# Performance work log

Hardware: AMD Instinct MI355X
Metric: run time of the kernel (lower is better)

## Reference

```python
import jax, jax.numpy as jnp
import numpy as np

EPS = 1e-5
GROUPS = 32
HEADS = 8
RES_SCALE = 0.7071067811865476  # 1/sqrt(2)


def group_norm(x, groups, weight=None, bias=None):
    # x: [b, c, t]; normalize over (c//groups, t) per group, like torch GroupNorm
    b, c, t = x.shape
    xg = x.reshape(b, groups, (c // groups) * t)
    mean = xg.mean(axis=-1, keepdims=True)
    var = xg.var(axis=-1, keepdims=True)
    xg = (xg - mean) * jax.lax.rsqrt(var + EPS)
    x = xg.reshape(b, c, t)
    if weight is not None:
        x = x * weight[None, :, None] + bias[None, :, None]
    return x


def setup_inputs() -> dict:
    key = jax.random.key(0)
    ks = jax.random.split(key, 7)
    b, c, hh, ww = 8, 512, 32, 32
    return {
        "x": jax.random.normal(ks[0], (b, c, hh, ww), dtype=jnp.float32),
        "gn_w": jax.random.uniform(ks[1], (c,), dtype=jnp.float32, minval=0.5, maxval=1.5),
        "gn_b": jax.random.normal(ks[2], (c,), dtype=jnp.float32) * 0.1,
        "qkv_w": jax.random.normal(ks[3], (3 * c, c), dtype=jnp.float32) * (c ** -0.5),
        "qkv_b": jax.random.normal(ks[4], (3 * c,), dtype=jnp.float32) * 0.02,
        "proj_w": jax.random.normal(ks[5], (c, c), dtype=jnp.float32) * 0.02,
        "proj_b": jax.random.normal(ks[6], (c,), dtype=jnp.float32) * 0.02,
    }


def reference(x, gn_w, gn_b, qkv_w, qkv_b, proj_w, proj_b):
    b, c, hh, ww = x.shape
    t = hh * ww
    ch = c // HEADS
    xf = x.reshape(b, c, t)
    xn = group_norm(xf, GROUPS, gn_w, gn_b)
    # 1x1 conv -> GEMM: [b, 3c, t]
    qkv = jnp.einsum('oc,bct->bot', qkv_w, xn) + qkv_b[None, :, None]
    # split order: per head contiguous [q_ch; k_ch; v_ch]
    qkv = qkv.reshape(b * HEADS, 3 * ch, t)
    q, k, v = jnp.split(qkv, 3, axis=1)
    scale = ch ** -0.25
    w = jnp.einsum('bct,bcs->bts', q * scale, k * scale)
    w = jax.nn.softmax(w.astype(jnp.float32), axis=-1).astype(qkv.dtype)
    a = jnp.einsum('bts,bcs->bct', w, v).reshape(b, c, t)
    h = jnp.einsum('oc,bct->bot', proj_w, a) + proj_b[None, :, None]
    out = group_norm(RES_SCALE * xn + h, GROUPS)  # functional group_norm: no affine
    return out.reshape(b, c, hh, ww)
```

## Files before the change

### kernel.cpp

```cpp
#include <hip/hip_runtime.h>


typedef unsigned short u16;
typedef __attribute__((ext_vector_type(8))) short short8v;
typedef __attribute__((ext_vector_type(4))) float float4v;

constexpr int NB = 8, NC = 512, NT = 1024, CPG = 16;
#define EPSV 1e-5f
#define RES_SCALE 0.7071067811865476f
#define QK_SCALE 0.35355339059327376f
#define LOG2E 1.4426950408889634f

static __device__ __forceinline__ u16 f2bf(float f) {
  unsigned int u = __builtin_bit_cast(unsigned int, f);
  u = (u + 0x7fffu + ((u >> 16) & 1u)) >> 16;
  return (u16)u;
}
static __device__ __forceinline__ float exp2_fast(float x) {
  float r;
  asm("v_exp_f32 %0, %1" : "=v"(r) : "v"(x));
  return r;
}
static __device__ __forceinline__ unsigned cvt_pk_bf16(float lo, float hi) {
  unsigned r;
  asm("v_cvt_pk_bf16_f32 %0, %1, %2" : "=v"(r) : "v"(lo), "v"(hi));
  return r;
}

__global__ __launch_bounds__(256) void gn1_prep_kernel(
    const float* __restrict__ x, const float* __restrict__ gw,
    const float* __restrict__ gb, float* __restrict__ xn, u16* __restrict__ xbt,
    const float* __restrict__ qw, const float* __restrict__ pw,
    u16* __restrict__ qwb, u16* __restrict__ pwb)
{
  __shared__ __attribute__((aligned(16))) u16 T[1024 * 24];
  __shared__ float rs[4], rq[4], stats[2];
  const int blk = blockIdx.x;
  const int tid = threadIdx.x;
  if (blk >= 256) {
    const int i = (blk - 256) * 256 + tid;
    const float* in; u16* out; int j;
    if (i < 98304) { in = qw; out = qwb; j = i; }
    else           { in = pw; out = pwb; j = i - 98304; }
    const float4 a = *(const float4*)(in + (size_t)j * 8);
    const float4 b = *(const float4*)(in + (size_t)j * 8 + 4);
    short8v o;
    o[0] = (short)f2bf(a.x); o[1] = (short)f2bf(a.y);
    o[2] = (short)f2bf(a.z); o[3] = (short)f2bf(a.w);
    o[4] = (short)f2bf(b.x); o[5] = (short)f2bf(b.y);
    o[6] = (short)f2bf(b.z); o[7] = (short)f2bf(b.w);
    *(short8v*)(out + (size_t)j * 8) = o;
    return;
  }
  const int b = blk >> 5, g = blk & 31;
  const size_t off = ((size_t)(b * NC + g * CPG)) * NT;
  const float4* s4 = (const float4*)(x + off);
  float sum = 0.f, sq = 0.f;
  #pragma unroll 4
  for (int i = tid; i < CPG * NT / 4; i += 256) {
    float4 v = s4[i];
    sum += v.x + v.y + v.z + v.w;
    sq  += v.x * v.x + v.y * v.y + v.z * v.z + v.w * v.w;
  }
  #pragma unroll
  for (int off2 = 32; off2; off2 >>= 1) {
    sum += __shfl_xor(sum, off2);
    sq  += __shfl_xor(sq,  off2);
  }
  const int wave = tid >> 6, lane = tid & 63;
  if (lane == 0) { rs[wave] = sum; rq[wave] = sq; }
  __syncthreads();
  if (tid == 0) {
    float S = rs[0] + rs[1] + rs[2] + rs[3];
    float Q = rq[0] + rq[1] + rq[2] + rq[3];
    float mean = S * (1.0f / (CPG * NT));
    float var  = Q * (1.0f / (CPG * NT)) - mean * mean;
    stats[0] = mean;
    stats[1] = rsqrtf(var + EPSV);
  }
  __syncthreads();
  const float mean = stats[0], rstd = stats[1];
  float4* d4 = (float4*)(xn + off);
  #pragma unroll 4
  for (int i = tid; i < CPG * NT / 4; i += 256) {
    const int ch = i >> 8;
    const float wv = gw[g * CPG + ch];
    const float a = rstd * wv;
    const float c2 = gb[g * CPG + ch] - mean * a;
    float4 v = s4[i];
    v.x = v.x * a + c2; v.y = v.y * a + c2;
    v.z = v.z * a + c2; v.w = v.w * a + c2;
    d4[i] = v;
    const int t4 = (i & 255) * 4;
    T[(t4 + 0) * 24 + ch] = f2bf(v.x);
    T[(t4 + 1) * 24 + ch] = f2bf(v.y);
    T[(t4 + 2) * 24 + ch] = f2bf(v.z);
    T[(t4 + 3) * 24 + ch] = f2bf(v.w);
  }
  __syncthreads();
  #pragma unroll
  for (int tt = 0; tt < 4; tt++) {
    const int t = tid + 256 * tt;
    uint4 lo = *(const uint4*)&T[t * 24];
    uint4 hi = *(const uint4*)&T[t * 24 + 8];
    u16* dst = xbt + ((size_t)b * NT + t) * NC + g * CPG;
    *(uint4*)dst = lo;
    *(uint4*)(dst + 8) = hi;
  }
}

template<int MODE>
__global__ __launch_bounds__(256) void mfma_gemm_kernel(
    const u16* __restrict__ Wb, const float* __restrict__ bias,
    const u16* __restrict__ Bt, u16* __restrict__ qkT,
    u16* __restrict__ vN, float* __restrict__ outF,
    const float* __restrict__ xnf)
{
  __shared__ __attribute__((aligned(16))) u16 lds[(MODE == 1) ? 17408 : 16384];
  const int tid = threadIdx.x;
  const int w = tid >> 6, l = tid & 63, lr = l & 15, lg = l >> 4;
  const int wm = (w >> 1) * 64, wn = (w & 1) * 64;
  const int bn = blockIdx.x * 128, bm = blockIdx.y * 128, b = blockIdx.z;

  const u16* Ag = Wb + (size_t)bm * 512;
  const u16* Bg = Bt + ((size_t)b * NT + bn) * 512;

  const int srow = w * 16 + (l >> 2);
  const int scg  = (l & 3) ^ ((l >> 3) & 3);
  const u16* ap0 = Ag + (size_t)srow * 512 + scg * 8;
  const u16* bp0 = Bg + (size_t)srow * 512 + scg * 8;
  char* ldsb = (char*)lds;
  char* adst0 = ldsb + w * 1024;

  float4v acc[4][4];
  #pragma unroll
  for (int i = 0; i < 4; i++)
    #pragma unroll
    for (int j = 0; j < 4; j++) acc[i][j] = (float4v){0.f, 0.f, 0.f, 0.f};

  #pragma unroll
  for (int r = 0; r < 2; r++) {
    __builtin_amdgcn_global_load_lds(ap0 + r * 64 * 512, adst0 + r * 4096, 16, 0, 0);
    __builtin_amdgcn_global_load_lds(bp0 + r * 64 * 512, adst0 + 8192 + r * 4096, 16, 0, 0);
  }
  asm volatile("s_waitcnt vmcnt(0)" ::: "memory");
  __builtin_amdgcn_s_barrier();

  for (int ks = 0; ks < 16; ++ks) {
    const int buf = ks & 1;
    if (ks < 15) {
      const size_t k0n = (size_t)(ks + 1) * 32;
      char* an = ldsb + (buf ^ 1) * 16384 + w * 1024;
      #pragma unroll
      for (int r = 0; r < 2; r++) {
        __builtin_amdgcn_global_load_lds(ap0 + k0n + r * 64 * 512, an + r * 4096, 16, 0, 0);
        __builtin_amdgcn_global_load_lds(bp0 + k0n + r * 64 * 512, an + 8192 + r * 4096, 16, 0, 0);
      }
    }
    const u16* au = lds + buf * 8192;
    const u16* bu = au + 4096;
    short8v af[4], bf[4];
    #pragma unroll
    for (int mi = 0; mi < 4; mi++) {
      const int m = wm + mi * 16 + lr;
      af[mi] = *(const short8v*)(au + m * 32 + ((lg ^ ((m >> 1) & 3)) * 8));
    }
    #pragma unroll
    for (int ni = 0; ni < 4; ni++) {
      const int n = wn + ni * 16 + lr;
      bf[ni] = *(const short8v*)(bu + n * 32 + ((lg ^ ((n >> 1) & 3)) * 8));
    }
    #pragma unroll
    for (int mi = 0; mi < 4; mi++)
      #pragma unroll
      for (int ni = 0; ni < 4; ni++)
        acc[mi][ni] = __builtin_amdgcn_mfma_f32_16x16x32_bf16(af[mi], bf[ni], acc[mi][ni], 0, 0, 0);
    if (ks < 15) {
      asm volatile("s_waitcnt vmcnt(0)" ::: "memory");
      __builtin_amdgcn_s_barrier();
    }
  }

  if (MODE == 0) {
    #pragma unroll
    for (int mi = 0; mi < 4; mi++) {
      const int m0 = bm + wm + mi * 16 + lg * 4;
      const int head = m0 / 192;
      const int r0 = m0 - head * 192;
      const float4 bv4 = *(const float4*)(bias + m0);
      if (r0 < 128) {
        const float scl = (r0 < 64) ? QK_SCALE * LOG2E : QK_SCALE;
        const int col = head * 128 + r0;
        #pragma unroll
        for (int ni = 0; ni < 4; ni++) {
          const int t = bn + wn + ni * 16 + lr;
          unsigned int lo = (unsigned)f2bf((acc[mi][ni][0] + bv4.x) * scl) |
                            ((unsigned)f2bf((acc[mi][ni][1] + bv4.y) * scl) << 16);
          unsigned int hi = (unsigned)f2bf((acc[mi][ni][2] + bv4.z) * scl) |
                            ((unsigned)f2bf((acc[mi][ni][3] + bv4.w) * scl) << 16);
          *(uint2*)(qkT + ((size_t)b * NT + t) * 1024 + col) = make_uint2(lo, hi);
        }
      } else {
        const int vc = head * 64 + (r0 - 128);
        #pragma unroll
        for (int ni = 0; ni < 4; ni++) {
          const int t = bn + wn + ni * 16 + lr;
          vN[((size_t)b * NC + vc + 0) * NT + t] = f2bf(acc[mi][ni][0] + bv4.x);
          vN[((size_t)b * NC + vc + 1) * NT + t] = f2bf(acc[mi][ni][1] + bv4.y);
          vN[((size_t)b * NC + vc + 2) * NT + t] = f2bf(acc[mi][ni][2] + bv4.z);
          vN[((size_t)b * NC + vc + 3) * NT + t] = f2bf(acc[mi][ni][3] + bv4.w);
        }
      }
    }
  } else {
    float* Cs = (float*)lds;
    for (int ph = 0; ph < 2; ph++) {
      __syncthreads();
      if ((w >> 1) == ph) {
        #pragma unroll
        for (int mi = 0; mi < 4; mi++)
          #pragma unroll
          for (int ni = 0; ni < 4; ni++) {
            const int rr = mi * 16 + lg * 4;
            const int cc2 = wn + ni * 16 + lr;
            #pragma unroll
            for (int r = 0; r < 4; r++)
              Cs[(rr + r) * 136 + cc2] = acc[mi][ni][r];
          }
      }
      __syncthreads();
      const int mloc = tid >> 2;
      const int m = bm + ph * 64 + mloc;
      const float bv = bias[m];
      const int cb = (tid & 3) * 32;
      const float* cr = Cs + mloc * 136 + cb;
      const float* xr = xnf + ((size_t)b * NC + m) * NT + bn + cb;
      float* yr = outF + ((size_t)b * NC + m) * NT + bn + cb;
      #pragma unroll
      for (int j = 0; j < 8; j++) {
        float4 c4 = *(const float4*)(cr + j * 4);
        float4 x4 = *(const float4*)(xr + j * 4);
        float4 o;
        o.x = c4.x + bv + RES_SCALE * x4.x;
        o.y = c4.y + bv + RES_SCALE * x4.y;
        o.z = c4.z + bv + RES_SCALE * x4.z;
        o.w = c4.w + bv + RES_SCALE * x4.w;
        *(float4*)(yr + j * 4) = o;
      }
    }
  }
}

__global__ __launch_bounds__(256) void groupnorm2_kernel(float* __restrict__ dst0)
{
  const int tid = threadIdx.x;
  const int b = blockIdx.x >> 5;
  const int g = blockIdx.x & 31;
  const size_t off = ((size_t)(b * NC + g * CPG)) * NT;
  float* dst = dst0 + off;
  const float4* s4 = (const float4*)dst;
  float sum = 0.f, sq = 0.f;
  #pragma unroll 4
  for (int i = tid; i < CPG * NT / 4; i += 256) {
    float4 v = s4[i];
    sum += v.x + v.y + v.z + v.w;
    sq  += v.x * v.x + v.y * v.y + v.z * v.z + v.w * v.w;
  }
  #pragma unroll
  for (int off2 = 32; off2; off2 >>= 1) {
    sum += __shfl_xor(sum, off2);
    sq  += __shfl_xor(sq,  off2);
  }
  __shared__ float rs[4], rq[4], stats[2];
  const int wave = tid >> 6, lane = tid & 63;
  if (lane == 0) { rs[wave] = sum; rq[wave] = sq; }
  __syncthreads();
  if (tid == 0) {
    float S = rs[0] + rs[1] + rs[2] + rs[3];
    float Q = rq[0] + rq[1] + rq[2] + rq[3];
    float mean = S * (1.0f / (CPG * NT));
    float var  = Q * (1.0f / (CPG * NT)) - mean * mean;
    stats[0] = mean;
    stats[1] = rsqrtf(var + EPSV);
  }
  __syncthreads();
  const float mean = stats[0], rstd = stats[1];
  float4* d4 = (float4*)dst;
  #pragma unroll 4
  for (int i = tid; i < CPG * NT / 4; i += 256) {
    float4 v = s4[i];
    const float c2 = -mean * rstd;
    v.x = v.x * rstd + c2; v.y = v.y * rstd + c2;
    v.z = v.z * rstd + c2; v.w = v.w * rstd + c2;
    d4[i] = v;
  }
}

__global__ __launch_bounds__(256, 4) void attn_mfma_kernel(
    const u16* __restrict__ qkT, const u16* __restrict__ vN, u16* __restrict__ aT)
{
  __shared__ __attribute__((aligned(16))) u16 lds[5 * 4096];
  const int tid = threadIdx.x;
  const int w = tid >> 6, l = tid & 63, lr = l & 15, lg = l >> 4;
  const int L = blockIdx.x;
  const int bh = (L & 7) * 8 + ((L >> 3) & 7);
  const int t0 = (L >> 6) * 64;
  const int b = bh >> 3, h = bh & 7;

  const u16* qbase = qkT + (size_t)b * NT * 1024 + h * 128;
  const u16* kbase = qbase + 64;
  const u16* vbase = vN + ((size_t)b * NC + h * 64) * NT;

  const size_t qrow = (size_t)(t0 + w * 16 + lr) * 1024;
  const short8v qa0 = *(const short8v*)(qbase + qrow + lg * 8);
  const short8v qa1 = *(const short8v*)(qbase + qrow + 32 + lg * 8);

  const int strow = w * 8 + (l >> 3);
  const int scg = (l & 7) ^ (l >> 3);
  const u16* kp0 = kbase + (size_t)strow * 1024 + scg * 8;
  const u16* vp0 = vbase + (size_t)strow * 1024 + scg * 8;
  char* ldsb = (char*)lds;
  u16* Psw = lds + 16384 + (w * 16 + lr) * 64;
  const int sx = (lr & 7) << 3;

  float4v out[4];
  #pragma unroll
  for (int nc = 0; nc < 4; nc++) out[nc] = (float4v){0.f, 0.f, 0.f, 0.f};
  float psum = 0.f;

  #pragma unroll
  for (int r = 0; r < 2; r++) {
    __builtin_amdgcn_global_load_lds(kp0 + (size_t)r * 32 * 1024,
                                     ldsb + w * 1024 + r * 4096, 16, 0, 0);
    __builtin_amdgcn_global_load_lds(vp0 + (size_t)r * 32 * 1024,
                                     ldsb + 16384 + w * 1024 + r * 4096, 16, 0, 0);
  }
  asm volatile("s_waitcnt vmcnt(0)" ::: "memory");
  __builtin_amdgcn_s_barrier();

  for (int it = 0; it < 16; ++it) {
    const int buf = it & 1;
    if (it < 15) {
      const size_t s0n = (size_t)(it + 1) * 64;
      char* kd = ldsb + (buf ^ 1) * 8192 + w * 1024;
      char* vd = ldsb + 16384 + (buf ^ 1) * 8192 + w * 1024;
      #pragma unroll
      for (int r = 0; r < 2; r++) {
        __builtin_amdgcn_global_load_lds(kp0 + (s0n + r * 32) * 1024, kd + r * 4096, 16, 0, 0);
        __builtin_amdgcn_global_load_lds(vp0 + s0n + (size_t)r * 32 * 1024, vd + r * 4096, 16, 0, 0);
      }
    }
    const u16* Kc = lds + buf * 4096;
    const u16* Vc = lds + 8192 + buf * 4096;

    float4v sacc[4];
    #pragma unroll
    for (int n = 0; n < 4; n++) sacc[n] = (float4v){0.f, 0.f, 0.f, 0.f};
    __builtin_amdgcn_s_setprio(1);
    #pragma unroll
    for (int n = 0; n < 4; n++) {
      const int srow = n * 16 + lr;
      short8v kb0 = *(const short8v*)(Kc + srow * 64 + ((lg ^ (srow & 7)) * 8));
      short8v kb1 = *(const short8v*)(Kc + srow * 64 + (((4 + lg) ^ (srow & 7)) * 8));
      sacc[n] = __builtin_amdgcn_mfma_f32_16x16x32_bf16(kb0, qa0, sacc[n], 0, 0, 0);
      sacc[n] = __builtin_amdgcn_mfma_f32_16x16x32_bf16(kb1, qa1, sacc[n], 0, 0, 0);
    }
    __builtin_amdgcn_s_setprio(0);

    #pragma unroll
    for (int n = 0; n < 4; n++) {
      float p0 = exp2_fast(sacc[n][0]);
      float p1 = exp2_fast(sacc[n][1]);
      float p2 = exp2_fast(sacc[n][2]);
      float p3 = exp2_fast(sacc[n][3]);
      psum += (p0 + p1) + (p2 + p3);
      unsigned w0 = cvt_pk_bf16(p0, p1);
      unsigned w1 = cvt_pk_bf16(p2, p3);
      *(uint2*)(Psw + ((n * 16 + lg * 4) ^ sx)) = make_uint2(w0, w1);
    }

    __builtin_amdgcn_s_setprio(1);
    #pragma unroll
    for (int kc = 0; kc < 2; kc++) {
      short8v pb = *(const short8v*)(Psw + ((kc * 32 + lg * 8) ^ sx));
      #pragma unroll
      for (int nc = 0; nc < 4; nc++) {
        const int crow = nc * 16 + lr;
        short8v vb = *(const short8v*)(Vc + crow * 64 + (((kc * 4 + lg) ^ (crow & 7)) * 8));
        out[nc] = __builtin_amdgcn_mfma_f32_16x16x32_bf16(vb, pb, out[nc], 0, 0, 0);
      }
    }
    __builtin_amdgcn_s_setprio(0);

    if (it < 15) {
      asm volatile("s_waitcnt vmcnt(0)" ::: "memory");
      __builtin_amdgcn_s_barrier();
    }
  }

  psum += __shfl_xor(psum, 16);
  psum += __shfl_xor(psum, 32);
  const float inv = 1.0f / psum;

  __syncthreads();
  u16* At = lds;
  #pragma unroll
  for (int nc = 0; nc < 4; nc++) {
    unsigned w0 = cvt_pk_bf16(out[nc][0] * inv, out[nc][1] * inv);
    unsigned w1 = cvt_pk_bf16(out[nc][2] * inv, out[nc][3] * inv);
    *(uint2*)(At + (w * 16 + lr) * 80 + nc * 16 + lg * 4) = make_uint2(w0, w1);
  }
  __syncthreads();
  const int t = tid >> 2, cp = (tid & 3) * 2;
  u16* dst = aT + ((size_t)b * NT + t0 + t) * NC + h * 64;
  #pragma unroll
  for (int q = 0; q < 2; q++)
    *(short8v*)(dst + (cp + q) * 8) = *(const short8v*)(At + t * 80 + (cp + q) * 8);
}

extern "C" void kernel_launch(void* const* d_in, const int* in_sizes, int n_in,
                              void* d_out, int out_size, void* d_ws, size_t ws_size,
                              hipStream_t stream)
{
  const float* x      = (const float*)d_in[0];
  const float* gn_w   = (const float*)d_in[1];
  const float* gn_b   = (const float*)d_in[2];
  const float* qkv_w  = (const float*)d_in[3];
  const float* qkv_b  = (const float*)d_in[4];
  const float* proj_w = (const float*)d_in[5];
  const float* proj_b = (const float*)d_in[6];
  float* out = (float*)d_out;

  float* xn  = (float*)d_ws;
  u16* base16 = (u16*)(xn + (size_t)NB * NC * NT);
  u16* xbt = base16;
  u16* qkT = xbt + (size_t)NB * NT * NC;
  u16* vN  = qkT + (size_t)NB * NT * 1024;
  u16* aT  = vN + (size_t)NB * NC * NT;
  u16* qwb = aT + (size_t)NB * NT * NC;
  u16* pwb = qwb + 1536 * 512;

  gn1_prep_kernel<<<dim3(768), 256, 0, stream>>>(x, gn_w, gn_b, xn, xbt,
                                                 qkv_w, proj_w, qwb, pwb);
  mfma_gemm_kernel<0><<<dim3(8, 12, NB), 256, 0, stream>>>(qwb, qkv_b, xbt, qkT, vN, nullptr, nullptr);
  attn_mfma_kernel<<<dim3(1024), 256, 0, stream>>>(qkT, vN, aT);
  mfma_gemm_kernel<1><<<dim3(8, 4, NB), 256, 0, stream>>>(pwb, proj_b, aT, nullptr, nullptr, out, xn);
  groupnorm2_kernel<<<dim3(256), 256, 0, stream>>>(out);
}
```

Baseline: 159.9 us.

## Store residual xn in bf16 and widen attention blocks to 512 threads

The normalized input kept for the residual is now written as bf16 instead of fp32. This halves the write traffic in the first groupnorm kernel and the residual read traffic in the projection epilogue. The attention kernel now uses 512-thread blocks covering 128 query rows, so each K/V tile loaded into LDS is shared by twice as many waves and the grid is halved. The cost is some precision loss in the residual term and higher per-block register and LDS pressure under the new launch bounds. The epilogue and tail code after the attention main loop were not visible, so their consistency with the new tile size cannot be confirmed.

```diff
diff --git a/kernel.cpp b/kernel.cpp
--- a/kernel.cpp
+++ b/kernel.cpp
@@ -16,6 +16,10 @@
   u = (u + 0x7fffu + ((u >> 16) & 1u)) >> 16;
   return (u16)u;
 }
+static __device__ __forceinline__ float bf2f(short s) {
+  unsigned u = ((unsigned)(unsigned short)s) << 16;
+  return __builtin_bit_cast(float, u);
+}
 static __device__ __forceinline__ float exp2_fast(float x) {
   float r;
   asm("v_exp_f32 %0, %1" : "=v"(r) : "v"(x));
@@ -29,7 +33,7 @@
 
 __global__ __launch_bounds__(256) void gn1_prep_kernel(
     const float* __restrict__ x, const float* __restrict__ gw,
-    const float* __restrict__ gb, float* __restrict__ xn, u16* __restrict__ xbt,
+    const float* __restrict__ gb, u16* __restrict__ xnc, u16* __restrict__ xbt,
     const float* __restrict__ qw, const float* __restrict__ pw,
     u16* __restrict__ qwb, u16* __restrict__ pwb)
 {
@@ -80,7 +84,6 @@
   }
   __syncthreads();
   const float mean = stats[0], rstd = stats[1];
-  float4* d4 = (float4*)(xn + off);
   #pragma unroll 4
   for (int i = tid; i < CPG * NT / 4; i += 256) {
     const int ch = i >> 8;
@@ -90,7 +93,8 @@
     float4 v = s4[i];
     v.x = v.x * a + c2; v.y = v.y * a + c2;
     v.z = v.z * a + c2; v.w = v.w * a + c2;
-    d4[i] = v;
+    *(uint2*)(xnc + off + (size_t)i * 4) =
+        make_uint2(cvt_pk_bf16(v.x, v.y), cvt_pk_bf16(v.z, v.w));
     const int t4 = (i & 255) * 4;
     T[(t4 + 0) * 24 + ch] = f2bf(v.x);
     T[(t4 + 1) * 24 + ch] = f2bf(v.y);
@@ -114,7 +118,7 @@
     const u16* __restrict__ Wb, const float* __restrict__ bias,
     const u16* __restrict__ Bt, u16* __restrict__ qkT,
     u16* __restrict__ vN, float* __restrict__ outF,
-    const float* __restrict__ xnf)
+    const u16* __restrict__ xnc)
 {
   __shared__ __attribute__((aligned(16))) u16 lds[(MODE == 1) ? 17408 : 16384];
   const int tid = threadIdx.x;
@@ -234,18 +238,24 @@
       const float bv = bias[m];
       const int cb = (tid & 3) * 32;
       const float* cr = Cs + mloc * 136 + cb;
-      const float* xr = xnf + ((size_t)b * NC + m) * NT + bn + cb;
+      const u16* xr = xnc + ((size_t)b * NC + m) * NT + bn + cb;
       float* yr = outF + ((size_t)b * NC + m) * NT + bn + cb;
       #pragma unroll
-      for (int j = 0; j < 8; j++) {
-        float4 c4 = *(const float4*)(cr + j * 4);
-        float4 x4 = *(const float4*)(xr + j * 4);
-        float4 o;
-        o.x = c4.x + bv + RES_SCALE * x4.x;
-        o.y = c4.y + bv + RES_SCALE * x4.y;
-        o.z = c4.z + bv + RES_SCALE * x4.z;
-        o.w = c4.w + bv + RES_SCALE * x4.w;
-        *(float4*)(yr + j * 4) = o;
+      for (int j = 0; j < 4; j++) {
+        short8v x8 = *(const short8v*)(xr + j * 8);
+        float4 c0 = *(const float4*)(cr + j * 8);
+        float4 c1 = *(const float4*)(cr + j * 8 + 4);
+        float4 o0, o1;
+        o0.x = c0.x + bv + RES_SCALE * bf2f(x8[0]);
+        o0.y = c0.y + bv + RES_SCALE * bf2f(x8[1]);
+        o0.z = c0.z + bv + RES_SCALE * bf2f(x8[2]);
+        o0.w = c0.w + bv + RES_SCALE * bf2f(x8[3]);
+        o1.x = c1.x + bv + RES_SCALE * bf2f(x8[4]);
+        o1.y = c1.y + bv + RES_SCALE * bf2f(x8[5]);
+        o1.z = c1.z + bv + RES_SCALE * bf2f(x8[6]);
+        o1.w = c1.w + bv + RES_SCALE * bf2f(x8[7]);
+        *(float4*)(yr + j * 8) = o0;
+        *(float4*)(yr + j * 8 + 4) = o1;
       }
     }
   }
@@ -296,15 +306,15 @@
   }
 }
 
-__global__ __launch_bounds__(256, 4) void attn_mfma_kernel(
+__global__ __launch_bounds__(512, 6) void attn_mfma_kernel(
     const u16* __restrict__ qkT, const u16* __restrict__ vN, u16* __restrict__ aT)
 {
-  __shared__ __attribute__((aligned(16))) u16 lds[5 * 4096];
+  __shared__ __attribute__((aligned(16))) u16 lds[24576];
   const int tid = threadIdx.x;
   const int w = tid >> 6, l = tid & 63, lr = l & 15, lg = l >> 4;
   const int L = blockIdx.x;
   const int bh = (L & 7) * 8 + ((L >> 3) & 7);
-  const int t0 = (L >> 6) * 64;
+  const int t0 = (L >> 6) * 128;
   const int b = bh >> 3, h = bh & 7;
 
   const u16* qbase = qkT + (size_t)b * NT * 1024 + h * 128;
@@ -315,10 +325,10 @@
   const short8v qa0 = *(const short8v*)(qbase + qrow + lg * 8);
   const short8v qa1 = *(const short8v*)(qbase + qrow + 32 + lg * 8);
 
-  const int strow = w * 8 + (l >> 3);
-  const int scg = (l & 7) ^ (l >> 3);
+  const int strow = tid >> 3;
+  const int scg = (tid & 7) ^ (strow & 7);
   const u16* kp0 = kbase + (size_t)strow * 1024 + scg * 8;
-  const u16* vp0 = vbase + (size_t)strow * 1024 + scg * 8;
+  const u16* vp0 = vbase + (size_t)strow * NT + scg * 8;
   char* ldsb = (char*)lds;
   u16* Psw = lds + 16384 + (w * 16 + lr) * 64;
   const int sx = (lr & 7) << 3;
@@ -328,13 +338,8 @@
   for (int nc = 0; nc < 4; nc++) out[nc] = (float4v){0.f, 0.f, 0.f, 0.f};
   float psum = 0.f;
 
-  #pragma unroll
-  for (int r = 0; r < 2; r++) {
-    __builtin_amdgcn_global_load_lds(kp0 + (size_t)r * 32 * 1024,
-                                     ldsb + w * 1024 + r * 4096, 16, 0, 0);
-    __builtin_amdgcn_global_load_lds(vp0 + (size_t)r * 32 * 1024,
-                                     ldsb + 16384 + w * 1024 + r * 4096, 16, 0, 0);
-  }
+  __builtin_amdgcn_global_load_lds(kp0, ldsb + tid * 16, 16, 0, 0);
+  __builtin_amdgcn_global_load_lds(vp0, ldsb + 16384 + tid * 16, 16, 0, 0);
   asm volatile("s_waitcnt vmcnt(0)" ::: "memory");
   __builtin_amdgcn_s_barrier();
 
@@ -342,13 +347,10 @@
     const int buf = it & 1;
     if (it < 15) {
       const size_t s0n = (size_t)(it + 1) * 64;
-      char* kd = ldsb + (buf ^ 1) * 8192 + w * 1024;
-      char* vd = ldsb + 16384 + (buf ^ 1) * 8192 + w * 1024;
-      #pragma unroll
-      for (int r = 0; r < 2; r++) {
-        __builtin_amdgcn_global_load_lds(kp0 + (s0n + r * 32) * 1024, kd + r * 4096, 16, 0, 0);
-        __builtin_amdgcn_global_load_lds(vp0 + s0n + (size_t)r * 32 * 1024, vd + r * 4096, 16, 0, 0);
-      }
+      __builtin_amdgcn_global_load_lds(kp0 + s0n * 1024,
+                                       ldsb + (buf ^ 1) * 8192 + tid * 16, 16, 0, 0);
+      __builtin_amdgcn_global_load_lds(vp0 + s0n,
+                                       ldsb + 16384 + (buf ^ 1) * 8192 + tid * 16, 16, 0, 0);
     }
     const u16* Kc = lds + buf * 4096;
     const u16* Vc = lds + 8192 + buf * 4096;
@@ -431,19 +433,18 @@
   const float* proj_b = (const float*)d_in[6];
   float* out = (float*)d_out;
 
-  float* xn  = (float*)d_ws;
-  u16* base16 = (u16*)(xn + (size_t)NB * NC * NT);
-  u16* xbt = base16;
-  u16* qkT = xbt + (size_t)NB * NT * NC;
+  u16* xbt = (u16*)d_ws;
+  u16* xnc = xbt + (size_t)NB * NT * NC;
+  u16* qkT = xnc + (size_t)NB * NC * NT;
   u16* vN  = qkT + (size_t)NB * NT * 1024;
   u16* aT  = vN + (size_t)NB * NC * NT;
   u16* qwb = aT + (size_t)NB * NT * NC;
   u16* pwb = qwb + 1536 * 512;
 
-  gn1_prep_kernel<<<dim3(768), 256, 0, stream>>>(x, gn_w, gn_b, xn, xbt,
+  gn1_prep_kernel<<<dim3(768), 256, 0, stream>>>(x, gn_w, gn_b, xnc, xbt,
                                                  qkv_w, proj_w, qwb, pwb);
   mfma_gemm_kernel<0><<<dim3(8, 12, NB), 256, 0, stream>>>(qwb, qkv_b, xbt, qkT, vN, nullptr, nullptr);
-  attn_mfma_kernel<<<dim3(1024), 256, 0, stream>>>(qkT, vN, aT);
-  mfma_gemm_kernel<1><<<dim3(8, 4, NB), 256, 0, stream>>>(pwb, proj_b, aT, nullptr, nullptr, out, xn);
+  attn_mfma_kernel<<<dim3(512), 512, 0, stream>>>(qkT, vN, aT);
+  mfma_gemm_kernel<1><<<dim3(8, 4, NB), 256, 0, stream>>>(pwb, proj_b, aT, nullptr, nullptr, out, xnc);
   groupnorm2_kernel<<<dim3(256), 256, 0, stream>>>(out);
 }
```

After: 159.0 us. No clear change (-0.5%).
